# Kernel optimization log

Hardware: AMD Instinct MI355X
Metric: run time of the kernel (lower is better)

## Reference

```python
import jax, jax.numpy as jnp
import numpy as np


def setup_inputs() -> dict:
    key = jax.random.key(0)
    ks = jax.random.split(key, 9)
    B, S, H, W = 4, 4096, 16, 16
    D = 256  # input_size == H*W == d_model
    sc = 1.0 / np.sqrt(D)
    return {
        "x": jax.random.normal(ks[0], (B, S, H, W), dtype=jnp.float32),
        "Wq": jax.random.normal(ks[1], (D, D), dtype=jnp.float32) * sc,
        "bq": jax.random.normal(ks[2], (D,), dtype=jnp.float32) * 0.01,
        "Wk": jax.random.normal(ks[3], (D, D), dtype=jnp.float32) * sc,
        "bk": jax.random.normal(ks[4], (D,), dtype=jnp.float32) * 0.01,
        "Wv": jax.random.normal(ks[5], (D, D), dtype=jnp.float32) * sc,
        "bv": jax.random.normal(ks[6], (D,), dtype=jnp.float32) * 0.01,
        "Wo": jax.random.normal(ks[7], (D, D), dtype=jnp.float32) * sc,
        "bo": jax.random.normal(ks[8], (D,), dtype=jnp.float32) * 0.01,
    }


def reference(x, Wq, bq, Wk, bk, Wv, bv, Wo, bo):
    B, S, H, W = x.shape
    xf = x.reshape(B, S, H * W)                      # [B, S, input_size]
    # nn.Linear: y = x @ W^T + b, weight shape [out, in]
    q = jax.nn.softplus(xf @ Wq.T + bq)              # [B, S, d]
    k = jax.nn.softplus(xf @ Wk.T + bk)              # [B, S, d]
    v = xf @ Wv.T + bv                               # [B, S, d]
    # naive ordering as in original: [B,S,S] scores, no softmax/normalization
    weight = jnp.einsum('bcd,bhd->bch', q, k)        # [B, S, S]
    result = jnp.einsum('bch,bhd->bcd', weight, v)   # [B, S, d]
    out = result @ Wo.T + bo                         # [B, S, input_size]
    return out.reshape(B, S, H, W)
```

## Files before the change

kernel.cpp:

```cpp
#include <hip/hip_runtime.h>
#include <hip/hip_bf16.h>
#include <math.h>

typedef __bf16 bf16_t;
typedef __bf16 bf16x8 __attribute__((ext_vector_type(8)));
typedef __bf16 bf16x4 __attribute__((ext_vector_type(4)));
typedef float  f32x4  __attribute__((ext_vector_type(4)));

#define NBATCH 4
#define SB     4096
#define BS     (NBATCH*SB)
#define DIM    256


__device__ __forceinline__ float softplus_f(float x) {
  return fmaxf(x, 0.0f) + log1pf(__expf(-fabsf(x)));
}

__device__ __forceinline__ void gload_lds16(const void* g, void* l) {
  __builtin_amdgcn_global_load_lds(
      (const __attribute__((address_space(1))) void*)g,
      (__attribute__((address_space(3))) void*)l,
      16, 0, 0);
}

__device__ __forceinline__ void cvt4(const float* __restrict__ s,
                                     bf16_t* __restrict__ d, int qi) {
  const float4 v = *(const float4*)(s + (size_t)qi * 4);
  bf16x4 o;
  o[0] = (bf16_t)v.x; o[1] = (bf16_t)v.y; o[2] = (bf16_t)v.z; o[3] = (bf16_t)v.w;
  *(bf16x4*)(d + (size_t)qi * 4) = o;
}


__global__ void prep_convert(const float* __restrict__ x,
                             const float* __restrict__ Wq,
                             const float* __restrict__ Wk,
                             bf16_t* __restrict__ xb,
                             bf16_t* __restrict__ Wqb,
                             bf16_t* __restrict__ Wkb,
                             float* __restrict__ MT) {
  const int QX = BS * DIM / 4;
  const int QW = DIM * DIM / 4;
  const int QM = NBATCH * DIM * DIM / 4;
  const int total = QX + 2 * QW + QM;
  for (int qi = blockIdx.x * blockDim.x + threadIdx.x; qi < total;
       qi += gridDim.x * blockDim.x) {
    if (qi < QX)               cvt4(x,  xb,  qi);
    else if (qi < QX + QW)     cvt4(Wq, Wqb, qi - QX);
    else if (qi < QX + 2 * QW) cvt4(Wk, Wkb, qi - QX - QW);
    else {
      float4 z; z.x = z.y = z.z = z.w = 0.0f;
      *(float4*)(MT + (size_t)(qi - QX - 2 * QW) * 4) = z;
    }
  }
}

__global__ void prep_wvo(const float* __restrict__ Wv,
                         const float* __restrict__ Wo,
                         const float* __restrict__ bv,
                         bf16_t* __restrict__ Wvob,
                         float* __restrict__ bvo) {
  const int j = blockIdx.x;
  const int t = threadIdx.x;
  float acc = 0.0f;
  for (int i = 0; i < DIM; ++i)
    acc = fmaf(Wo[j * DIM + i], Wv[i * DIM + t], acc);
  Wvob[(size_t)j * DIM + t] = (bf16_t)acc;
  if (t == 0) {
    float a = 0.0f;
    for (int i = 0; i < DIM; ++i) a = fmaf(Wo[j * DIM + i], bv[i], a);
    bvo[j] = a;
  }
}

__device__ __forceinline__ void gemm128_core(
    const bf16_t* __restrict__ Abase,
    const bf16_t* __restrict__ Bbase,
    char* smem, int tid, f32x4 acc[4][4]) {
  const int lane = tid & 63;
  const int w = tid >> 6;
  const int wr = w & 1, wc = w >> 1;
  #pragma unroll
  for (int kk = 0; kk < 2; ++kk) {
    const char* asrc = (const char*)Abase + kk * 256;
    const char* bsrc = (const char*)Bbase + kk * 256;
    #pragma unroll
    for (int it = 0; it < 8; ++it) {
      const int L = it * 256 + tid;
      const int row = L >> 4;
      const int lch = (L & 15) ^ (row & 7);
      char* la = smem + (size_t)(it * 256 + w * 64) * 16;
      char* lb = la + 32768;
      gload_lds16(asrc + (size_t)row * 512 + lch * 16, la);
      gload_lds16(bsrc + (size_t)row * 512 + lch * 16, lb);
    }
    __syncthreads();
    #pragma unroll
    for (int ks = 0; ks < 4; ++ks) {
      const int kb = ks * 64 + ((lane >> 4) << 4);
      bf16x8 af[4], bg[4];
      #pragma unroll
      for (int mi = 0; mi < 4; ++mi) {
        const int row = wr * 64 + mi * 16 + (lane & 15);
        const int ch = (kb >> 4) ^ (row & 7);
        af[mi] = *(const bf16x8*)(smem + (size_t)row * 256 + ch * 16);
      }
      #pragma unroll
      for (int ni = 0; ni < 4; ++ni) {
        const int row = wc * 64 + ni * 16 + (lane & 15);
        const int ch = (kb >> 4) ^ (row & 7);
        bg[ni] = *(const bf16x8*)(smem + 32768 + (size_t)row * 256 + ch * 16);
      }
      #pragma unroll
      for (int mi = 0; mi < 4; ++mi)
        #pragma unroll
        for (int ni = 0; ni < 4; ++ni)
          acc[mi][ni] = __builtin_amdgcn_mfma_f32_16x16x32_bf16(
              af[mi], bg[ni], acc[mi][ni], 0, 0, 0);
    }
    __syncthreads();
  }
}

__global__ __launch_bounds__(256) void qkv_gemm(
    const bf16_t* __restrict__ xb,
    const bf16_t* __restrict__ Wqb,
    const bf16_t* __restrict__ Wkb,
    const bf16_t* __restrict__ Wvob,
    const float* __restrict__ bq,
    const float* __restrict__ bk,
    const float* __restrict__ bvo,
    bf16_t* __restrict__ qo,
    bf16_t* __restrict__ kT,
    bf16_t* __restrict__ vT) {
  __shared__ __align__(16) char smem[65536];
  const int mode = blockIdx.z;
  const int r0 = blockIdx.x * 128;
  const int c0 = blockIdx.y * 128;
  const bf16_t* W   = (mode == 0) ? Wqb : (mode == 1) ? Wkb : Wvob;
  const float* bias = (mode == 0) ? bq  : (mode == 1) ? bk  : bvo;
  const int tid = threadIdx.x;
  const int lane = tid & 63;
  const int w = tid >> 6;
  const int wr = w & 1, wc = w >> 1;

  f32x4 zero = {0.0f, 0.0f, 0.0f, 0.0f};
  f32x4 acc[4][4];
  #pragma unroll
  for (int i = 0; i < 4; ++i)
    #pragma unroll
    for (int j = 0; j < 4; ++j) acc[i][j] = zero;

  gemm128_core(xb + (size_t)r0 * DIM, W + (size_t)c0 * DIM, smem, tid, acc);

  const int batch = r0 >> 12;
  #pragma unroll
  for (int ni = 0; ni < 4; ++ni) {
    const int col = c0 + wc * 64 + ni * 16 + (lane & 15);
    const float bb = bias[col];
    #pragma unroll
    for (int mi = 0; mi < 4; ++mi) {
      const int srow = r0 + wr * 64 + mi * 16 + ((lane >> 4) << 2);
      f32x4 v = acc[mi][ni];
      float o0 = v[0] + bb, o1 = v[1] + bb, o2 = v[2] + bb, o3 = v[3] + bb;
      if (mode < 2) {
        o0 = softplus_f(o0); o1 = softplus_f(o1);
        o2 = softplus_f(o2); o3 = softplus_f(o3);
      }
      if (mode == 0) {
        qo[(size_t)(srow + 0) * DIM + col] = (bf16_t)o0;
        qo[(size_t)(srow + 1) * DIM + col] = (bf16_t)o1;
        qo[(size_t)(srow + 2) * DIM + col] = (bf16_t)o2;
        qo[(size_t)(srow + 3) * DIM + col] = (bf16_t)o3;
      } else {
        bf16_t* dst = (mode == 1) ? kT : vT;
        const int sin = srow & (SB - 1);
        bf16x4 p;
        p[0] = (bf16_t)o0; p[1] = (bf16_t)o1; p[2] = (bf16_t)o2; p[3] = (bf16_t)o3;
        *(bf16x4*)(dst + (size_t)batch * DIM * SB + (size_t)col * SB + sin) = p;
      }
    }
  }
}

__global__ __launch_bounds__(256) void m_gemm(
    const bf16_t* __restrict__ kT,
    const bf16_t* __restrict__ vT,
    float* __restrict__ MT) {
  const int quad = blockIdx.x;
  const int sc   = blockIdx.y;
  const int b    = blockIdx.z;
  const int tid = threadIdx.x;
  const int lane = tid & 63;
  const int w = tid >> 6;
  const int wr = w & 1, wc = w >> 1;
  const int j0 = (quad & 1) * 128 + wr * 64;
  const int d0 = (quad >> 1) * 128 + wc * 64;
  const bf16_t* vb = vT + (size_t)b * DIM * SB;
  const bf16_t* kb = kT + (size_t)b * DIM * SB;

  f32x4 zero = {0.0f, 0.0f, 0.0f, 0.0f};
  f32x4 acc[4][4];
  #pragma unroll
  for (int i = 0; i < 4; ++i)
    #pragma unroll
    for (int j = 0; j < 4; ++j) acc[i][j] = zero;

  const int svec = sc * 128 + ((lane >> 4) << 3);
  #pragma unroll
  for (int it = 0; it < 4; ++it) {
    const int s = svec + it * 32;
    bf16x8 af[4], bg[4];
    #pragma unroll
    for (int mi = 0; mi < 4; ++mi)
      af[mi] = *(const bf16x8*)(vb + (size_t)(j0 + mi * 16 + (lane & 15)) * SB + s);
    #pragma unroll
    for (int ni = 0; ni < 4; ++ni)
      bg[ni] = *(const bf16x8*)(kb + (size_t)(d0 + ni * 16 + (lane & 15)) * SB + s);
    #pragma unroll
    for (int mi = 0; mi < 4; ++mi)
      #pragma unroll
      for (int ni = 0; ni < 4; ++ni)
        acc[mi][ni] = __builtin_amdgcn_mfma_f32_16x16x32_bf16(
            af[mi], bg[ni], acc[mi][ni], 0, 0, 0);
  }

  float* o = MT + (size_t)b * DIM * DIM;
  #pragma unroll
  for (int mi = 0; mi < 4; ++mi) {
    const int row = j0 + mi * 16 + ((lane >> 4) << 2);
    #pragma unroll
    for (int ni = 0; ni < 4; ++ni) {
      const int col = d0 + ni * 16 + (lane & 15);
      #pragma unroll
      for (int r = 0; r < 4; ++r)
        atomicAdd(o + (size_t)(row + r) * DIM + col, acc[mi][ni][r]);
    }
  }
}

__global__ void conv_nt(const float* __restrict__ MT, bf16_t* __restrict__ NTb) {
  const int qi = blockIdx.x * blockDim.x + threadIdx.x;
  if (qi < NBATCH * DIM * DIM / 4) {
    const float4 v = *(const float4*)(MT + (size_t)qi * 4);
    bf16x4 o;
    o[0] = (bf16_t)v.x; o[1] = (bf16_t)v.y; o[2] = (bf16_t)v.z; o[3] = (bf16_t)v.w;
    *(bf16x4*)(NTb + (size_t)qi * 4) = o;
  }
}

__global__ __launch_bounds__(256) void out_gemm(
    const bf16_t* __restrict__ qo,
    const bf16_t* __restrict__ NTb,
    const float* __restrict__ bo,
    float* __restrict__ out) {
  __shared__ __align__(16) char smem[65536];
  const int r0 = blockIdx.x * 128;
  const int c0 = blockIdx.y * 128;
  const int batch = r0 >> 12;
  const int tid = threadIdx.x;
  const int lane = tid & 63;
  const int w = tid >> 6;
  const int wr = w & 1, wc = w >> 1;

  f32x4 zero = {0.0f, 0.0f, 0.0f, 0.0f};
  f32x4 acc[4][4];
  #pragma unroll
  for (int i = 0; i < 4; ++i)
    #pragma unroll
    for (int j = 0; j < 4; ++j) acc[i][j] = zero;

  gemm128_core(qo + (size_t)r0 * DIM,
               NTb + (size_t)batch * DIM * DIM + (size_t)c0 * DIM,
               smem, tid, acc);

  #pragma unroll
  for (int ni = 0; ni < 4; ++ni) {
    const int col = c0 + wc * 64 + ni * 16 + (lane & 15);
    const float bb = bo[col];
    #pragma unroll
    for (int mi = 0; mi < 4; ++mi) {
      const int srow = r0 + wr * 64 + mi * 16 + ((lane >> 4) << 2);
      f32x4 v = acc[mi][ni];
      #pragma unroll
      for (int r = 0; r < 4; ++r)
        out[(size_t)(srow + r) * DIM + col] = v[r] + bb;
    }
  }
}


extern "C" void kernel_launch(void* const* d_in, const int* in_sizes, int n_in,
                              void* d_out, int out_size, void* d_ws, size_t ws_size,
                              hipStream_t stream) {
  const float* x  = (const float*)d_in[0];
  const float* Wq = (const float*)d_in[1];
  const float* bq = (const float*)d_in[2];
  const float* Wk = (const float*)d_in[3];
  const float* bk = (const float*)d_in[4];
  const float* Wv = (const float*)d_in[5];
  const float* bv = (const float*)d_in[6];
  const float* Wo = (const float*)d_in[7];
  const float* bo = (const float*)d_in[8];
  float* out = (float*)d_out;

  char* ws = (char*)d_ws;
  bf16_t* xb   = (bf16_t*)(ws);
  bf16_t* qo   = (bf16_t*)(ws + 8388608);
  bf16_t* kT   = (bf16_t*)(ws + 16777216);
  bf16_t* vT   = (bf16_t*)(ws + 25165824);
  bf16_t* Wqb  = (bf16_t*)(ws + 33554432);
  bf16_t* Wkb  = (bf16_t*)(ws + 33685504);
  bf16_t* Wvob = (bf16_t*)(ws + 33816576);
  float*  bvo  = (float*)(ws + 33947648);
  float*  MT   = (float*)(ws + 33948672);
  bf16_t* NTb  = (bf16_t*)(ws + 34997248);

  prep_convert<<<1024, 256, 0, stream>>>(x, Wq, Wk, xb, Wqb, Wkb, MT);
  prep_wvo<<<256, 256, 0, stream>>>(Wv, Wo, bv, Wvob, bvo);
  qkv_gemm<<<dim3(128, 2, 3), 256, 0, stream>>>(xb, Wqb, Wkb, Wvob,
                                                bq, bk, bvo, qo, kT, vT);
  m_gemm<<<dim3(4, 32, 4), 256, 0, stream>>>(kT, vT, MT);
  conv_nt<<<256, 256, 0, stream>>>(MT, NTb);
  out_gemm<<<dim3(128, 2), 256, 0, stream>>>(qo, NTb, bo, out);
}
```

Baseline: 176.7 us.

## Replace atomic split-K accumulation with partial buffers and fused reduce; merge prep kernels

m_gemm now gives each block a 256-long sequence chunk instead of 128 (16 chunks instead of 32) and writes its partial 256x256 result with plain stores into a per-chunk buffer, instead of atomically adding into a zeroed accumulator. A reduce kernel sums the 16 partials and converts to bf16, replacing the old convert kernel. The two prep kernels are merged into one launch, and the accumulator zeroing is dropped. This removes atomic contention and one launch, at the cost of a 16 MB partial buffer that must be written and read back, plus half as many m_gemm blocks.

New measurement: 149.6 us. -15.3%, faster.

```diff
diff --git a/kernel.cpp b/kernel.cpp
--- a/kernel.cpp
+++ b/kernel.cpp
@@ -11,6 +11,7 @@
 #define SB     4096
 #define BS     (NBATCH*SB)
 #define DIM    256
+#define NCHUNK 16
 
 
 __device__ __forceinline__ float softplus_f(float x) {
@@ -32,45 +33,39 @@
   *(bf16x4*)(d + (size_t)qi * 4) = o;
 }
 
-
-__global__ void prep_convert(const float* __restrict__ x,
-                             const float* __restrict__ Wq,
-                             const float* __restrict__ Wk,
-                             bf16_t* __restrict__ xb,
-                             bf16_t* __restrict__ Wqb,
-                             bf16_t* __restrict__ Wkb,
-                             float* __restrict__ MT) {
-  const int QX = BS * DIM / 4;
-  const int QW = DIM * DIM / 4;
-  const int QM = NBATCH * DIM * DIM / 4;
-  const int total = QX + 2 * QW + QM;
-  for (int qi = blockIdx.x * blockDim.x + threadIdx.x; qi < total;
-       qi += gridDim.x * blockDim.x) {
-    if (qi < QX)               cvt4(x,  xb,  qi);
-    else if (qi < QX + QW)     cvt4(Wq, Wqb, qi - QX);
-    else if (qi < QX + 2 * QW) cvt4(Wk, Wkb, qi - QX - QW);
-    else {
-      float4 z; z.x = z.y = z.z = z.w = 0.0f;
-      *(float4*)(MT + (size_t)(qi - QX - 2 * QW) * 4) = z;
-    }
-  }
-}
-
-__global__ void prep_wvo(const float* __restrict__ Wv,
+__global__ void prep_all(const float* __restrict__ x,
+                         const float* __restrict__ Wq,
+                         const float* __restrict__ Wk,
+                         const float* __restrict__ Wv,
                          const float* __restrict__ Wo,
                          const float* __restrict__ bv,
+                         bf16_t* __restrict__ xb,
+                         bf16_t* __restrict__ Wqb,
+                         bf16_t* __restrict__ Wkb,
                          bf16_t* __restrict__ Wvob,
                          float* __restrict__ bvo) {
-  const int j = blockIdx.x;
-  const int t = threadIdx.x;
-  float acc = 0.0f;
-  for (int i = 0; i < DIM; ++i)
-    acc = fmaf(Wo[j * DIM + i], Wv[i * DIM + t], acc);
-  Wvob[(size_t)j * DIM + t] = (bf16_t)acc;
-  if (t == 0) {
-    float a = 0.0f;
-    for (int i = 0; i < DIM; ++i) a = fmaf(Wo[j * DIM + i], bv[i], a);
-    bvo[j] = a;
+  if (blockIdx.x < 1024) {
+    const int QX = BS * DIM / 4;
+    const int QW = DIM * DIM / 4;
+    const int total = QX + 2 * QW;
+    for (int qi = blockIdx.x * blockDim.x + threadIdx.x; qi < total;
+         qi += 1024 * blockDim.x) {
+      if (qi < QX)           cvt4(x,  xb,  qi);
+      else if (qi < QX + QW) cvt4(Wq, Wqb, qi - QX);
+      else                   cvt4(Wk, Wkb, qi - QX - QW);
+    }
+  } else {
+    const int j = blockIdx.x - 1024;
+    const int t = threadIdx.x;
+    float acc = 0.0f;
+    for (int i = 0; i < DIM; ++i)
+      acc = fmaf(Wo[j * DIM + i], Wv[i * DIM + t], acc);
+    Wvob[(size_t)j * DIM + t] = (bf16_t)acc;
+    if (t == 0) {
+      float a = 0.0f;
+      for (int i = 0; i < DIM; ++i) a = fmaf(Wo[j * DIM + i], bv[i], a);
+      bvo[j] = a;
+    }
   }
 }
 
@@ -187,7 +182,7 @@
 __global__ __launch_bounds__(256) void m_gemm(
     const bf16_t* __restrict__ kT,
     const bf16_t* __restrict__ vT,
-    float* __restrict__ MT) {
+    float* __restrict__ MTp) {
   const int quad = blockIdx.x;
   const int sc   = blockIdx.y;
   const int b    = blockIdx.z;
@@ -207,9 +202,9 @@
     #pragma unroll
     for (int j = 0; j < 4; ++j) acc[i][j] = zero;
 
-  const int svec = sc * 128 + ((lane >> 4) << 3);
-  #pragma unroll
-  for (int it = 0; it < 4; ++it) {
+  const int svec = sc * 256 + ((lane >> 4) << 3);
+  #pragma unroll
+  for (int it = 0; it < 8; ++it) {
     const int s = svec + it * 32;
     bf16x8 af[4], bg[4];
     #pragma unroll
@@ -226,7 +221,7 @@
             af[mi], bg[ni], acc[mi][ni], 0, 0, 0);
   }
 
-  float* o = MT + (size_t)b * DIM * DIM;
+  float* o = MTp + ((size_t)sc * NBATCH + b) * DIM * DIM;
   #pragma unroll
   for (int mi = 0; mi < 4; ++mi) {
     const int row = j0 + mi * 16 + ((lane >> 4) << 2);
@@ -235,19 +230,25 @@
       const int col = d0 + ni * 16 + (lane & 15);
       #pragma unroll
       for (int r = 0; r < 4; ++r)
-        atomicAdd(o + (size_t)(row + r) * DIM + col, acc[mi][ni][r]);
-    }
-  }
-}
-
-__global__ void conv_nt(const float* __restrict__ MT, bf16_t* __restrict__ NTb) {
+        o[(size_t)(row + r) * DIM + col] = acc[mi][ni][r];
+    }
+  }
+}
+
+__global__ void reduce_nt(const float* __restrict__ MTp,
+                          bf16_t* __restrict__ NTb) {
   const int qi = blockIdx.x * blockDim.x + threadIdx.x;
-  if (qi < NBATCH * DIM * DIM / 4) {
-    const float4 v = *(const float4*)(MT + (size_t)qi * 4);
-    bf16x4 o;
-    o[0] = (bf16_t)v.x; o[1] = (bf16_t)v.y; o[2] = (bf16_t)v.z; o[3] = (bf16_t)v.w;
-    *(bf16x4*)(NTb + (size_t)qi * 4) = o;
-  }
+  f32x4 s = {0.0f, 0.0f, 0.0f, 0.0f};
+  #pragma unroll
+  for (int c = 0; c < NCHUNK; ++c) {
+    const float4 v =
+        *(const float4*)(MTp + (size_t)c * NBATCH * DIM * DIM + (size_t)qi * 4);
+    s[0] += v.x; s[1] += v.y; s[2] += v.z; s[3] += v.w;
+  }
+  bf16x4 o;
+  o[0] = (bf16_t)s[0]; o[1] = (bf16_t)s[1];
+  o[2] = (bf16_t)s[2]; o[3] = (bf16_t)s[3];
+  *(bf16x4*)(NTb + (size_t)qi * 4) = o;
 }
 
 __global__ __launch_bounds__(256) void out_gemm(
@@ -314,14 +315,14 @@
   bf16_t* Wkb  = (bf16_t*)(ws + 33685504);
   bf16_t* Wvob = (bf16_t*)(ws + 33816576);
   float*  bvo  = (float*)(ws + 33947648);
-  float*  MT   = (float*)(ws + 33948672);
-  bf16_t* NTb  = (bf16_t*)(ws + 34997248);
-
-  prep_convert<<<1024, 256, 0, stream>>>(x, Wq, Wk, xb, Wqb, Wkb, MT);
-  prep_wvo<<<256, 256, 0, stream>>>(Wv, Wo, bv, Wvob, bvo);
+  bf16_t* NTb  = (bf16_t*)(ws + 33948672);
+  float*  MTp  = (float*)(ws + 34472960);
+
+  prep_all<<<1280, 256, 0, stream>>>(x, Wq, Wk, Wv, Wo, bv,
+                                     xb, Wqb, Wkb, Wvob, bvo);
   qkv_gemm<<<dim3(128, 2, 3), 256, 0, stream>>>(xb, Wqb, Wkb, Wvob,
                                                 bq, bk, bvo, qo, kT, vT);
-  m_gemm<<<dim3(4, 32, 4), 256, 0, stream>>>(kT, vT, MT);
-  conv_nt<<<256, 256, 0, stream>>>(MT, NTb);
+  m_gemm<<<dim3(4, NCHUNK, 4), 256, 0, stream>>>(kT, vT, MTp);
+  reduce_nt<<<256, 256, 0, stream>>>(MTp, NTb);
   out_gemm<<<dim3(128, 2), 256, 0, stream>>>(qo, NTb, bo, out);
 }
```
